# Performance work log

Measured on AMD Instinct MI355X. Metric: run time of the kernel, lower is better.

## Reference

```python
import jax, jax.numpy as jnp
import numpy as np

ALPHA = 0.1
K_HOPS = 16


def mlp_readout(y, ws, bs):
    # MLPReadout with L=2: two relu layers then linear
    for w, b in zip(ws[:-1], bs[:-1]):
        y = jax.nn.relu(y @ w.T + b)
    return y @ ws[-1].T + bs[-1]


def gru_dir(xs, w_ih, w_hh, b_ih, b_hh, reverse):
    # xs: [B, T, D]; PyTorch GRU cell semantics
    H = w_hh.shape[1]
    def cell(h, xt):
        gi = xt @ w_ih.T + b_ih            # [B, 3H]
        gh = h @ w_hh.T + b_hh             # [B, 3H]
        i_r, i_z, i_n = jnp.split(gi, 3, -1)
        h_r, h_z, h_n = jnp.split(gh, 3, -1)
        r = jax.nn.sigmoid(i_r + h_r)
        z = jax.nn.sigmoid(i_z + h_z)
        n = jnp.tanh(i_n + r * h_n)
        h2 = (1.0 - z) * n + z * h
        return h2, h2
    h0 = jnp.zeros((xs.shape[0], H), xs.dtype)
    _, ys = jax.lax.scan(cell, h0, jnp.swapaxes(xs, 0, 1), reverse=reverse)
    return jnp.swapaxes(ys, 0, 1)          # [B, T, H]


def appnp(x, edge_index):
    # APPNP with GCN symmetric normalization and self-loops
    N = x.shape[0]
    loop = jnp.arange(N, dtype=edge_index.dtype)
    src = jnp.concatenate([edge_index[0], loop])
    dst = jnp.concatenate([edge_index[1], loop])
    deg = jax.ops.segment_sum(jnp.ones(src.shape, x.dtype), dst, num_segments=N)
    dinv = jax.lax.rsqrt(jnp.maximum(deg, 1.0))
    w = (dinv[src] * dinv[dst])[:, None]    # [E+N, 1]
    def step(z, _):
        m = jax.ops.segment_sum(z[src] * w, dst, num_segments=N)
        return (1.0 - ALPHA) * m + ALPHA * x, None
    z, _ = jax.lax.scan(step, x, None, length=K_HOPS)
    return z


def setup_inputs():
    key = jax.random.key(0)
    ks = jax.random.split(key, 24)
    N, D, E, B, T, S, Hs, C = 20000, 768, 200000, 64, 128, 128, 512, 14
    sc = 0.05
    p = {}
    p['x'] = jax.random.normal(ks[0], (N, D), jnp.float32)
    p['edge_index'] = jax.random.randint(ks[1], (2, E), 0, N, dtype=jnp.int32).astype(jnp.int64)
    p['sequence'] = jax.random.normal(ks[2], (B, T, S), jnp.float32)
    p['batch'] = jnp.sort(jax.random.randint(ks[3], (N,), 0, B, dtype=jnp.int32)).astype(jnp.int64)
    # BiGRU params (forward / backward directions)
    p['gru_wih_f'] = jax.random.normal(ks[4], (3 * Hs, S), jnp.float32) * sc
    p['gru_whh_f'] = jax.random.normal(ks[5], (3 * Hs, Hs), jnp.float32) * sc
    p['gru_bih_f'] = jax.random.normal(ks[6], (3 * Hs,), jnp.float32) * sc
    p['gru_bhh_f'] = jax.random.normal(ks[7], (3 * Hs,), jnp.float32) * sc
    p['gru_wih_b'] = jax.random.normal(ks[8], (3 * Hs, S), jnp.float32) * sc
    p['gru_whh_b'] = jax.random.normal(ks[9], (3 * Hs, Hs), jnp.float32) * sc
    p['gru_bih_b'] = jax.random.normal(ks[10], (3 * Hs,), jnp.float32) * sc
    p['gru_bhh_b'] = jax.random.normal(ks[11], (3 * Hs,), jnp.float32) * sc
    # mlp_graph: 768 -> 384 -> 192 -> 14
    p['mg_w0'] = jax.random.normal(ks[12], (384, 768), jnp.float32) * sc
    p['mg_b0'] = jnp.zeros((384,), jnp.float32)
    p['mg_w1'] = jax.random.normal(ks[13], (192, 384), jnp.float32) * sc
    p['mg_b1'] = jnp.zeros((192,), jnp.float32)
    p['mg_w2'] = jax.random.normal(ks[14], (C, 192), jnp.float32) * sc
    p['mg_b2'] = jnp.zeros((C,), jnp.float32)
    # mlp_seq: 1024 -> 512 -> 256 -> 14
    p['ms_w0'] = jax.random.normal(ks[15], (512, 1024), jnp.float32) * sc
    p['ms_b0'] = jnp.zeros((512,), jnp.float32)
    p['ms_w1'] = jax.random.normal(ks[16], (256, 512), jnp.float32) * sc
    p['ms_b1'] = jnp.zeros((256,), jnp.float32)
    p['ms_w2'] = jax.random.normal(ks[17], (C, 256), jnp.float32) * sc
    p['ms_b2'] = jnp.zeros((C,), jnp.float32)
    return p


def reference(x, edge_index, sequence, batch,
              gru_wih_f, gru_whh_f, gru_bih_f, gru_bhh_f,
              gru_wih_b, gru_whh_b, gru_bih_b, gru_bhh_b,
              mg_w0, mg_b0, mg_w1, mg_b1, mg_w2, mg_b2,
              ms_w0, ms_b0, ms_w1, ms_b1, ms_w2, ms_b2):
    B = sequence.shape[0]
    # BiGRU over sequence (dropout is identity in eval mode)
    fwd = gru_dir(sequence, gru_wih_f, gru_whh_f, gru_bih_f, gru_bhh_f, False)
    bwd = gru_dir(sequence, gru_wih_b, gru_whh_b, gru_bih_b, gru_bhh_b, True)
    seq_out = jnp.concatenate([fwd, bwd], axis=-1)   # [B, T, 2H]
    seq1 = jnp.mean(seq_out, axis=1)                 # avg_pool over time
    seq2 = jnp.max(seq_out, axis=1)                  # max_pool over time
    seq_logits = mlp_readout(seq1 + seq2, [ms_w0, ms_w1, ms_w2], [ms_b0, ms_b1, ms_b2])
    # APPNP K-hop sparse propagation + global mean pool
    z = appnp(x, edge_index)
    cnt = jnp.maximum(jax.ops.segment_sum(jnp.ones((x.shape[0],), x.dtype), batch, num_segments=B), 1.0)
    pooled = jax.ops.segment_sum(z, batch, num_segments=B) / cnt[:, None]
    g_logits = mlp_readout(pooled, [mg_w0, mg_w1, mg_w2], [mg_b0, mg_b1, mg_b2])
    return g_logits + seq_logits
```

## Files before the change

### kernel.cpp

```cpp
#include <hip/hip_runtime.h>
#include <stdint.h>

#define ALPHA 0.1f
#define NN 20000
#define DF 768
#define NE 200000
#define NB 64
#define TSEQ 128
#define SF 128
#define HS 512
#define NCLS 14

typedef __attribute__((ext_vector_type(8))) short short8;
typedef __attribute__((ext_vector_type(4))) float f32x4;
typedef __attribute__((ext_vector_type(4))) unsigned int u32x4;

#define OFF_DEG     0u
#define OFF_CSRC    80000u
#define OFF_CNTB    160000u
#define OFF_FLAG64  176640u
#define ZERO_INTS   44161u
#define OFF_ROWPTR  176896u
#define OFF_CURSOR  257024u
#define OFF_DINV    337024u
#define OFF_COL     417024u
#define OFF_WGT     1217024u
#define OFF_V0      2017280u
#define OFF_V1      7137280u
#define OFF_HBUF    12257280u
#define OFF_HFLAG   12519424u
#define OFF_YSEQ    12781568u
#define OFF_PART    13240320u

__device__ __forceinline__ unsigned short f2b(float f) {
  union { float f; unsigned u; } v; v.f = f;
  unsigned u = v.u;
  return (unsigned short)((u + 0x7FFFu + ((u >> 16) & 1u)) >> 16);
}

__device__ __forceinline__ int idx_at(const int* p, long long i, int mode64) {
  return mode64 ? p[2*i] : p[i];
}

__device__ __forceinline__ float dot4(float4 a, float4 b) {
  return a.x * b.x + a.y * b.y + a.z * b.z + a.w * b.w;
}

__global__ void zero2_kernel(int* p1, int n1, int* p2, int n2) {
  int i = blockIdx.x * blockDim.x + threadIdx.x;
  if (i < n1) p1[i] = 0;
  int j = i - n1;
  if (j >= 0 && j < n2) p2[j] = 0;
}

__global__ void detect_i64_kernel(const int* e, int* flag) {
  int lane = threadIdx.x;
  int ok = 1;
  for (int i = lane; i < 256; i += 64) ok &= (e[2 * i + 1] == 0);
  ok = __all(ok);
  if (lane == 0 && blockIdx.x == 0) *flag = ok ? 1 : 0;
}

__global__ void hist_kernel(const int* e, const int* batch, int* deg, int* csrc,
                            int* cntb, const int* flag) {
  int i = blockIdx.x * blockDim.x + threadIdx.x;
  int m = *flag;
  if (i < NE) {
    int s = idx_at(e, i, m);
    int d = idx_at(e, (long long)NE + i, m);
    atomicAdd(&csrc[s], 1);
    atomicAdd(&deg[d], 1);
  }
  if (i < NN) atomicAdd(&cntb[idx_at(batch, i, m)], 1);
}

__global__ __launch_bounds__(1024) void combo_kernel(
    const int* __restrict__ csrc, const int* __restrict__ deg,
    int* __restrict__ row_ptr, int* __restrict__ cursor,
    float* __restrict__ dinv, const int* __restrict__ batch,
    const int* __restrict__ flag, float* __restrict__ v0) {
  const int tid = threadIdx.x, b = blockIdx.x;
  if (b < 20) {
    __shared__ int sA[1024], sB[1024];
    __shared__ int wred[16];
    __shared__ int carry_s;
    int psum = 0;
    for (int i = tid; i < b * 1000; i += 1024) psum += csrc[i];
    for (int off = 1; off < 64; off <<= 1) psum += __shfl_xor(psum, off);
    if ((tid & 63) == 0) wred[tid >> 6] = psum;
    __syncthreads();
    if (tid == 0) {
      int c = 0;
#pragma unroll
      for (int w = 0; w < 16; ++w) c += wred[w];
      carry_s = c;
    }
    int i = b * 1000 + tid;
    int active = (tid < 1000);
    int v = active ? csrc[i] : 0;
    sA[tid] = v;
    __syncthreads();
    int carry = carry_s;
    int* src = sA; int* dst = sB;
    for (int off = 1; off < 1024; off <<= 1) {
      dst[tid] = src[tid] + (tid >= off ? src[tid - off] : 0);
      __syncthreads();
      int* t = src; src = dst; dst = t;
    }
    if (active) {
      int ex = carry + src[tid] - v;
      row_ptr[i] = ex; cursor[i] = ex;
      dinv[i] = rsqrtf((float)(deg[i] + 1));
    }
    if (b == 19 && tid == 0) row_ptr[NN] = carry + src[999];
  } else {
    int m = *flag;
    long long j = (long long)(b - 20) * 1024 + tid;
    if (j < (long long)NN * 64) {
      int n = (int)(j >> 6), gb = (int)(j & 63);
      v0[j] = (idx_at(batch, n, m) == gb) ? 1.0f : 0.0f;
    }
  }
}

__global__ void fill_kernel(const int* e, const float* dinv, int* cursor,
                            int* colA, float* wgt, const int* flag) {
  int i = blockIdx.x * blockDim.x + threadIdx.x;
  if (i >= NE) return;
  int m = *flag;
  int s = idx_at(e, i, m);
  int d = idx_at(e, (long long)NE + i, m);
  int pos = atomicAdd(&cursor[s], 1);
  colA[pos] = d;
  wgt[pos] = dinv[s] * dinv[d];
}

__global__ __launch_bounds__(256) void hop_kernel(
    const float* __restrict__ vin, float* __restrict__ vout,
    const int* __restrict__ row_ptr, const int* __restrict__ colA,
    const float* __restrict__ wgt, const float* __restrict__ dinv,
    const int* __restrict__ batch, const int* __restrict__ flag) {
  int wid = (blockIdx.x * blockDim.x + threadIdx.x) >> 6;
  int lane = threadIdx.x & 63;
  if (wid >= NN) return;
  const int quad = lane >> 4, l15 = lane & 15;
  const int c4 = l15 * 4;
  float di = dinv[wid];
  int e0 = __builtin_amdgcn_readfirstlane(row_ptr[wid]);
  int e1 = __builtin_amdgcn_readfirstlane(row_ptr[wid + 1]);

  float ax, ay, az, aw;
  {
    float w = (quad == 0) ? di * di : 0.0f;
    const float* vr = vin + (size_t)wid * 64 + c4;
    ax = w * vr[0]; ay = w * vr[1]; az = w * vr[2]; aw = w * vr[3];
  }
  for (int e = e0; e < e1; e += 16) {
    int i0 = e + quad, i1 = i0 + 4, i2 = i0 + 8, i3 = i0 + 12;
    int a0 = (i0 < e1), a1 = (i1 < e1), a2 = (i2 < e1), a3 = (i3 < e1);
    int j0 = a0 ? i0 : e0, j1 = a1 ? i1 : e0, j2 = a2 ? i2 : e0, j3 = a3 ? i3 : e0;
    int cc0 = colA[j0], cc1 = colA[j1], cc2 = colA[j2], cc3 = colA[j3];
    float w0 = a0 ? wgt[j0] : 0.0f, w1 = a1 ? wgt[j1] : 0.0f;
    float w2 = a2 ? wgt[j2] : 0.0f, w3 = a3 ? wgt[j3] : 0.0f;
    float4 v0 = *(const float4*)(vin + (size_t)cc0 * 64 + c4);
    float4 v1 = *(const float4*)(vin + (size_t)cc1 * 64 + c4);
    float4 v2 = *(const float4*)(vin + (size_t)cc2 * 64 + c4);
    float4 v3 = *(const float4*)(vin + (size_t)cc3 * 64 + c4);
    ax += w0 * v0.x + w1 * v1.x + w2 * v2.x + w3 * v3.x;
    ay += w0 * v0.y + w1 * v1.y + w2 * v2.y + w3 * v3.y;
    az += w0 * v0.z + w1 * v1.z + w2 * v2.z + w3 * v3.z;
    aw += w0 * v0.w + w1 * v1.w + w2 * v2.w + w3 * v3.w;
  }
  ax += __shfl_xor(ax, 16); ax += __shfl_xor(ax, 32);
  ay += __shfl_xor(ay, 16); ay += __shfl_xor(ay, 32);
  az += __shfl_xor(az, 16); az += __shfl_xor(az, 32);
  aw += __shfl_xor(aw, 16); aw += __shfl_xor(aw, 32);
  if (quad == 0) {
    int b = idx_at(batch, wid, *flag);
    float* o = vout + (size_t)wid * 64 + c4;
    float4 r;
    r.x = (1.0f - ALPHA) * ax + ((b == c4 + 0) ? ALPHA : 0.0f);
    r.y = (1.0f - ALPHA) * ay + ((b == c4 + 1) ? ALPHA : 0.0f);
    r.z = (1.0f - ALPHA) * az + ((b == c4 + 2) ? ALPHA : 0.0f);
    r.w = (1.0f - ALPHA) * aw + ((b == c4 + 3) ? ALPHA : 0.0f);
    *(float4*)o = r;
  }
}

__global__ __launch_bounds__(256) void spmm_kernel(
    const float* __restrict__ S, const float* __restrict__ x,
    float* __restrict__ partial) {
  __shared__ float red[4][64][17];
  int tid = threadIdx.x;
  int w = tid >> 6, lane = tid & 63;
  int beta = blockIdx.x;
  int ft = beta % 48, cg = beta / 48;
  int ch = cg * 4 + w;
  int f0 = ft * 16;
  int n0 = (ch * NN) >> 6, n1 = ((ch + 1) * NN) >> 6;
  float acc[16];
#pragma unroll
  for (int f = 0; f < 16; ++f) acc[f] = 0.0f;
  for (int n = n0; n < n1; ++n) {
    float sv = S[n * 64 + lane];
    const float4* xr = (const float4*)(x + (size_t)n * DF + f0);
    float4 x0 = xr[0], x1 = xr[1], x2 = xr[2], x3 = xr[3];
    acc[0] += sv * x0.x; acc[1] += sv * x0.y; acc[2] += sv * x0.z; acc[3] += sv * x0.w;
    acc[4] += sv * x1.x; acc[5] += sv * x1.y; acc[6] += sv * x1.z; acc[7] += sv * x1.w;
    acc[8] += sv * x2.x; acc[9] += sv * x2.y; acc[10] += sv * x2.z; acc[11] += sv * x2.w;
    acc[12] += sv * x3.x; acc[13] += sv * x3.y; acc[14] += sv * x3.z; acc[15] += sv * x3.w;
  }
#pragma unroll
  for (int f = 0; f < 16; ++f) red[w][lane][f] = acc[f];
  __syncthreads();
#pragma unroll
  for (int ff = 0; ff < 4; ++ff) {
    int f = w * 4 + ff;
    float s = red[0][lane][f] + red[1][lane][f] + red[2][lane][f] + red[3][lane][f];
    partial[((size_t)(cg * 64 + lane)) * DF + f0 + f] = s;
  }
}

__global__ __launch_bounds__(256) void mlp_seq_kernel(
    const float* __restrict__ y_seq,
    const float* __restrict__ w0, const float* __restrict__ b0,
    const float* __restrict__ w1, const float* __restrict__ b1,
    const float* __restrict__ w2, const float* __restrict__ b2,
    float* __restrict__ out) {
  __shared__ float a0[1024], h1[512], h2[256];
  const int tid = threadIdx.x, b = blockIdx.x;
  ((float4*)a0)[tid] = ((const float4*)(y_seq + (size_t)b * 1024))[tid];
  __syncthreads();
  {
    int n = tid * 2;
    float acc0 = b0[n], acc1 = b0[n + 1];
    const float4* wa = (const float4*)(w0 + (size_t)n * 1024);
    const float4* wb = wa + 256;
#pragma unroll 4
    for (int k = 0; k < 256; ++k) {
      float4 av = ((float4*)a0)[k];
      acc0 += dot4(av, wa[k]);
      acc1 += dot4(av, wb[k]);
    }
    h1[n] = fmaxf(acc0, 0.0f);
    h1[n + 1] = fmaxf(acc1, 0.0f);
  }
  __syncthreads();
  {
    float acc = b1[tid];
    const float4* wa = (const float4*)(w1 + (size_t)tid * 512);
#pragma unroll 4
    for (int k = 0; k < 128; ++k) acc += dot4(((float4*)h1)[k], wa[k]);
    h2[tid] = fmaxf(acc, 0.0f);
  }
  __syncthreads();
  if (tid < 224) {
    int o = tid >> 4, l = tid & 15;
    const float4* wa = (const float4*)(w2 + (size_t)o * 256);
    float part = 0.0f;
#pragma unroll
    for (int k = l; k < 64; k += 16) part += dot4(((float4*)h2)[k], wa[k]);
    part += __shfl_xor(part, 1); part += __shfl_xor(part, 2);
    part += __shfl_xor(part, 4); part += __shfl_xor(part, 8);
    if (l == 0) out[b * NCLS + o] = part + b2[o];
  }
}

__global__ __launch_bounds__(256) void mlp_graph_kernel(
    const float* __restrict__ partial, const int* __restrict__ cntb,
    const float* __restrict__ w0, const float* __restrict__ b0,
    const float* __restrict__ w1, const float* __restrict__ b1,
    const float* __restrict__ w2, const float* __restrict__ b2,
    float* __restrict__ out) {
  __shared__ float a0[768], h1[384], h2[192];
  const int tid = threadIdx.x, b = blockIdx.x;
  int cnt = cntb[b]; if (cnt < 1) cnt = 1;
  const float cinv = 1.0f / (float)cnt;
  if (tid < 192) {
    float4 s = {0, 0, 0, 0};
#pragma unroll
    for (int c = 0; c < 16; ++c) {
      float4 p = ((const float4*)(partial + ((size_t)(c * 64 + b)) * DF))[tid];
      s.x += p.x; s.y += p.y; s.z += p.z; s.w += p.w;
    }
    s.x *= cinv; s.y *= cinv; s.z *= cinv; s.w *= cinv;
    ((float4*)a0)[tid] = s;
  }
  __syncthreads();
  if (tid < 192) {
    int n = tid * 2;
    float acc0 = b0[n], acc1 = b0[n + 1];
    const float4* wa = (const float4*)(w0 + (size_t)n * 768);
    const float4* wb = wa + 192;
#pragma unroll 4
    for (int k = 0; k < 192; ++k) {
      float4 av = ((float4*)a0)[k];
      acc0 += dot4(av, wa[k]);
      acc1 += dot4(av, wb[k]);
    }
    h1[n] = fmaxf(acc0, 0.0f);
    h1[n + 1] = fmaxf(acc1, 0.0f);
  }
  __syncthreads();
  if (tid < 192) {
    float acc = b1[tid];
    const float4* wa = (const float4*)(w1 + (size_t)tid * 384);
#pragma unroll 4
    for (int k = 0; k < 96; ++k) acc += dot4(((float4*)h1)[k], wa[k]);
    h2[tid] = fmaxf(acc, 0.0f);
  }
  __syncthreads();
  if (tid < 224) {
    int o = tid >> 4, l = tid & 15;
    const float4* wa = (const float4*)(w2 + (size_t)o * 192);
    float part = 0.0f;
#pragma unroll
    for (int k = l; k < 48; k += 16) part += dot4(((float4*)h2)[k], wa[k]);
    part += __shfl_xor(part, 1); part += __shfl_xor(part, 2);
    part += __shfl_xor(part, 4); part += __shfl_xor(part, 8);
    if (l == 0) atomicAdd(&out[b * NCLS + o], part + b2[o]);
  }
}

__global__ __launch_bounds__(64, 1) void gru_kernel(
    const float* __restrict__ seq,
    const float* __restrict__ wih_f, const float* __restrict__ whh_f,
    const float* __restrict__ bih_f, const float* __restrict__ bhh_f,
    const float* __restrict__ wih_b, const float* __restrict__ whh_b,
    const float* __restrict__ bih_b, const float* __restrict__ bhh_b,
    unsigned* __restrict__ hbuf, unsigned* __restrict__ hflag,
    float* __restrict__ y_seq) {
  __shared__ unsigned short hl[8 * 648];

  const int lane = threadIdx.x;
  const int quad = lane >> 4, l15 = lane & 15;
  const int d  = blockIdx.x >> 8;
  const int g  = (blockIdx.x >> 5) & 7;
  const int rk = blockIdx.x & 31;
  const int seqbase = g * 8;
  const int c0 = rk * 16;

  const float* WHHd = d ? whh_b : whh_f;
  const float* WIHd = d ? wih_b : wih_f;
  const float* BIHd = d ? bih_b : bih_f;
  const float* BHHd = d ? bhh_b : bhh_f;

  auto ldw = [&](int gcol, int j) -> short8 {
    int k0 = j * 32 + quad * 8;
    const float* p = (k0 < 512) ? (WHHd + (size_t)gcol * 512 + k0)
                                : (WIHd + (size_t)gcol * 128 + (k0 - 512));
    float4 f0 = *(const float4*)p;
    float4 f1 = *(const float4*)(p + 4);
    short8 r;
    r[0] = (short)f2b(f0.x); r[1] = (short)f2b(f0.y);
    r[2] = (short)f2b(f0.z); r[3] = (short)f2b(f0.w);
    r[4] = (short)f2b(f1.x); r[5] = (short)f2b(f1.y);
    r[6] = (short)f2b(f1.z); r[7] = (short)f2b(f1.w);
    return r;
  };
  short8 wr[20], wz[20], wn[20];
#pragma unroll
  for (int j = 0; j < 20; ++j) {
    wr[j] = ldw(c0 + l15, j);
    wz[j] = ldw(512 + c0 + l15, j);
    wn[j] = ldw(1024 + c0 + l15, j);
  }

  auto stage_x = [&](int t_x) {
    int tt = d ? (127 - t_x) : t_x;
    int s = lane >> 3, k0 = (lane & 7) * 16;
    const float* sp = seq + (size_t)(seqbase + s) * (TSEQ * SF) + tt * SF + k0;
    float4 a = *(const float4*)sp;
    float4 b = *(const float4*)(sp + 4);
    float4 c = *(const float4*)(sp + 8);
    float4 e = *(const float4*)(sp + 12);
    unsigned* xq = (unsigned*)(hl + s * 648 + 512 + k0);
    xq[0] = (unsigned)f2b(a.x) | ((unsigned)f2b(a.y) << 16);
    xq[1] = (unsigned)f2b(a.z) | ((unsigned)f2b(a.w) << 16);
    xq[2] = (unsigned)f2b(b.x) | ((unsigned)f2b(b.y) << 16);
    xq[3] = (unsigned)f2b(b.z) | ((unsigned)f2b(b.w) << 16);
    xq[4] = (unsigned)f2b(c.x) | ((unsigned)f2b(c.y) << 16);
    xq[5] = (unsigned)f2b(c.z) | ((unsigned)f2b(c.w) << 16);
    xq[6] = (unsigned)f2b(e.x) | ((unsigned)f2b(e.y) << 16);
    xq[7] = (unsigned)f2b(e.z) | ((unsigned)f2b(e.w) << 16);
  };

  for (int i = lane; i < 8 * 512; i += 64)
    hl[(i >> 9) * 648 + (i & 511)] = 0;
  stage_x(0);

  const float b_r  = BIHd[c0 + l15] + BHHd[c0 + l15];
  const float b_z  = BIHd[512 + c0 + l15] + BHHd[512 + c0 + l15];
  const float b_in = BIHd[1024 + c0 + l15];
  const float b_hn = BHHd[1024 + c0 + l15];

  float hprev[4] = {0, 0, 0, 0};
  float msum[4]  = {0, 0, 0, 0};
  float mxv[4]   = {-1e30f, -1e30f, -1e30f, -1e30f};

  for (int t = 0; t < 128; ++t) {
    f32x4 ar = {0, 0, 0, 0}, az = {0, 0, 0, 0};
    f32x4 anh = {0, 0, 0, 0}, anx = {0, 0, 0, 0};
    const unsigned short* arow = hl + (l15 & 7) * 648 + quad * 8;
#pragma unroll
    for (int kc = 0; kc < 20; ++kc) {
      short8 af = *(const short8*)(arow + kc * 32);
      ar = __builtin_amdgcn_mfma_f32_16x16x32_bf16(af, wr[kc], ar, 0, 0, 0);
      az = __builtin_amdgcn_mfma_f32_16x16x32_bf16(af, wz[kc], az, 0, 0, 0);
      if (kc < 16)
        anh = __builtin_amdgcn_mfma_f32_16x16x32_bf16(af, wn[kc], anh, 0, 0, 0);
      else
        anx = __builtin_amdgcn_mfma_f32_16x16x32_bf16(af, wn[kc], anx, 0, 0, 0);
    }

    float h2v[4];
#pragma unroll
    for (int rr = 0; rr < 4; ++rr) {
      float r = 1.0f / (1.0f + __expf(-(ar[rr] + b_r)));
      float z = 1.0f / (1.0f + __expf(-(az[rr] + b_z)));
      float narg = anx[rr] + b_in + r * (anh[rr] + b_hn);
      float e2 = __expf(-2.0f * fabsf(narg));
      float nt = (1.0f - e2) / (1.0f + e2);
      nt = (narg < 0.0f) ? -nt : nt;
      float h2 = (1.0f - z) * nt + z * hprev[rr];
      hprev[rr] = h2; msum[rr] += h2; mxv[rr] = fmaxf(mxv[rr], h2);
      h2v[rr] = h2;
    }

    if (t < 127) {
      const int slot = (t + 1) & 1;
      const unsigned tag = (unsigned)(t + 1);
#pragma unroll
      for (int rr = 0; rr < 4; ++rr) {
        unsigned me = f2b(h2v[rr]);
        unsigned nb = (unsigned)__shfl_xor((int)me, 1);
        if (lane < 32 && !(lane & 1)) {
          int row = (lane >> 4) * 4 + rr;
          unsigned word = (me & 0xFFFFu) | (nb << 16);
          unsigned* dp = hbuf +
              ((size_t)((slot * 2 + d) * 64 + seqbase + row)) * 256 +
              (unsigned)((c0 + (lane & 15)) >> 1);
          asm volatile("global_store_dword %0, %1, off sc0 sc1"
                       :: "v"(dp), "v"(word) : "memory");
        }
      }
      asm volatile("s_waitcnt vmcnt(0)" ::: "memory");
      if (lane == 0) {
        unsigned* fpo = hflag + ((size_t)(slot * 2 + d) * 8 + g) * 64 + rk;
        unsigned tv = tag;
        asm volatile("global_store_dword %0, %1, off sc0 sc1"
                     :: "v"(fpo), "v"(tv) : "memory");
      }
      stage_x(t + 1);
      const unsigned* fp = hflag + ((size_t)(slot * 2 + d) * 8 + g) * 64 + (lane & 31);
      int guard = 0;
      unsigned fv;
      for (;;) {
        asm volatile("global_load_dword %0, %1, off sc0 sc1"
                     : "=v"(fv) : "v"(fp) : "memory");
        asm volatile("s_waitcnt vmcnt(0)" ::: "memory");
        __builtin_amdgcn_sched_barrier(0);
        if (__all(fv == tag)) break;
        if (++guard > (1 << 20)) break;
        __builtin_amdgcn_s_sleep(1);
      }
      const unsigned* db = hbuf + (size_t)((slot * 2 + d) * 64 + seqbase) * 256;
      u32x4 w[8];
#pragma unroll
      for (int c = 0; c < 8; ++c)
        asm volatile("global_load_dwordx4 %0, %1, off sc0 sc1"
                     : "=v"(w[c]) : "v"(db + c * 256 + lane * 4) : "memory");
      asm volatile("s_waitcnt vmcnt(0)" ::: "memory");
      __builtin_amdgcn_sched_barrier(0);
#pragma unroll
      for (int c = 0; c < 8; ++c) {
        unsigned* dp = (unsigned*)(hl + c * 648) + lane * 4;
        dp[0] = w[c][0]; dp[1] = w[c][1]; dp[2] = w[c][2]; dp[3] = w[c][3];
      }
    }
  }

  if (lane < 32) {
#pragma unroll
    for (int rr = 0; rr < 4; ++rr) {
      int row = (lane >> 4) * 4 + rr;
      y_seq[(size_t)(seqbase + row) * 1024 + d * 512 + c0 + l15] =
          msum[rr] * (1.0f / 128.0f) + mxv[rr];
    }
  }
}

extern "C" void kernel_launch(void* const* d_in, const int* in_sizes, int n_in,
                              void* d_out, int out_size, void* d_ws, size_t ws_size,
                              hipStream_t stream) {
  const float* x      = (const float*)d_in[0];
  const int*   eidx   = (const int*)d_in[1];
  const float* seq    = (const float*)d_in[2];
  const int*   batch  = (const int*)d_in[3];
  const float* wih_f  = (const float*)d_in[4];
  const float* whh_f  = (const float*)d_in[5];
  const float* bih_f  = (const float*)d_in[6];
  const float* bhh_f  = (const float*)d_in[7];
  const float* wih_b  = (const float*)d_in[8];
  const float* whh_b  = (const float*)d_in[9];
  const float* bih_b  = (const float*)d_in[10];
  const float* bhh_b  = (const float*)d_in[11];
  const float* mg_w0  = (const float*)d_in[12];
  const float* mg_b0  = (const float*)d_in[13];
  const float* mg_w1  = (const float*)d_in[14];
  const float* mg_b1  = (const float*)d_in[15];
  const float* mg_w2  = (const float*)d_in[16];
  const float* mg_b2  = (const float*)d_in[17];
  const float* ms_w0  = (const float*)d_in[18];
  const float* ms_b0  = (const float*)d_in[19];
  const float* ms_w1  = (const float*)d_in[20];
  const float* ms_b1  = (const float*)d_in[21];
  const float* ms_w2  = (const float*)d_in[22];
  const float* ms_b2  = (const float*)d_in[23];
  float* out = (float*)d_out;
  char* ws = (char*)d_ws;

  int*   deg     = (int*)(ws + OFF_DEG);
  int*   csrc    = (int*)(ws + OFF_CSRC);
  int*   cntb    = (int*)(ws + OFF_CNTB);
  int*   flag    = (int*)(ws + OFF_FLAG64);
  int*   row_ptr = (int*)(ws + OFF_ROWPTR);
  int*   cursor  = (int*)(ws + OFF_CURSOR);
  float* dinv    = (float*)(ws + OFF_DINV);
  int*   colA    = (int*)(ws + OFF_COL);
  float* wgtA    = (float*)(ws + OFF_WGT);
  float* V0      = (float*)(ws + OFF_V0);
  float* V1      = (float*)(ws + OFF_V1);
  unsigned* hbuf = (unsigned*)(ws + OFF_HBUF);
  unsigned* hflag= (unsigned*)(ws + OFF_HFLAG);
  float* y_seq   = (float*)(ws + OFF_YSEQ);
  float* part    = (float*)(ws + OFF_PART);

  zero2_kernel<<<(ZERO_INTS + 2048 + 255) / 256, 256, 0, stream>>>(
      (int*)ws, (int)ZERO_INTS, (int*)(ws + OFF_HFLAG), 2048);
  detect_i64_kernel<<<1, 64, 0, stream>>>(eidx, flag);
  hist_kernel<<<(NE + 255) / 256, 256, 0, stream>>>(eidx, batch, deg, csrc,
                                                    cntb, flag);
  combo_kernel<<<20 + (NN * 64 + 1023) / 1024, 1024, 0, stream>>>(
      csrc, deg, row_ptr, cursor, dinv, batch, flag, V0);
  fill_kernel<<<(NE + 255) / 256, 256, 0, stream>>>(eidx, dinv, cursor, colA, wgtA, flag);

  for (int h = 0; h < 16; ++h) {
    const float* vin = (h & 1) ? V1 : V0;
    float* vout = (h & 1) ? V0 : V1;
    hop_kernel<<<(NN * 64 + 255) / 256, 256, 0, stream>>>(vin, vout, row_ptr, colA,
                                                          wgtA, dinv, batch, flag);
  }

  spmm_kernel<<<768, 256, 0, stream>>>(V0, x, part);

  gru_kernel<<<512, 64, 0, stream>>>(
      seq, wih_f, whh_f, bih_f, bhh_f, wih_b, whh_b, bih_b, bhh_b, hbuf, hflag, y_seq);

  mlp_seq_kernel<<<64, 256, 0, stream>>>(y_seq, ms_w0, ms_b0, ms_w1, ms_b1,
                                         ms_w2, ms_b2, out);
  mlp_graph_kernel<<<64, 256, 0, stream>>>(part, cntb, mg_w0, mg_b0, mg_w1, mg_b1,
                                           mg_w2, mg_b2, out);
  (void)in_sizes; (void)n_in; (void)out_size; (void)ws_size;
}
```

Before: 1.228 ms.

## Store APPNP propagation vectors in fp16 and fuse spmm into GRU launch

The 64-wide propagated batch-indicator vectors are now stored as fp16 instead of fp32, halving the gather traffic of each of the 16 hop kernels. The spmm reduction is merged into the GRU kernel as extra blocks so both run concurrently in a single launch, letting the latency-bound GRU recurrence overlap the bandwidth-bound spmm. The fused launch uses 256-thread blocks, and the 512 GRU blocks keep only their first 64 threads. This risks precision loss in the propagated values and may disturb the GRU's cross-block flag synchronization if its blocks are not all co-resident.

```diff
diff --git a/kernel.cpp b/kernel.cpp
--- a/kernel.cpp
+++ b/kernel.cpp
@@ -38,6 +38,14 @@
   return (unsigned short)((u + 0x7FFFu + ((u >> 16) & 1u)) >> 16);
 }
 
+union U16h { unsigned short u; _Float16 h; };
+__device__ __forceinline__ float h2f(unsigned short u) {
+  U16h t; t.u = u; return (float)t.h;
+}
+__device__ __forceinline__ unsigned short f2h(float f) {
+  U16h t; t.h = (_Float16)f; return t.u;
+}
+
 __device__ __forceinline__ int idx_at(const int* p, long long i, int mode64) {
   return mode64 ? p[2*i] : p[i];
 }
@@ -78,7 +86,7 @@
     const int* __restrict__ csrc, const int* __restrict__ deg,
     int* __restrict__ row_ptr, int* __restrict__ cursor,
     float* __restrict__ dinv, const int* __restrict__ batch,
-    const int* __restrict__ flag, float* __restrict__ v0) {
+    const int* __restrict__ flag, unsigned short* __restrict__ v0) {
   const int tid = threadIdx.x, b = blockIdx.x;
   if (b < 20) {
     __shared__ int sA[1024], sB[1024];
@@ -118,7 +126,7 @@
     long long j = (long long)(b - 20) * 1024 + tid;
     if (j < (long long)NN * 64) {
       int n = (int)(j >> 6), gb = (int)(j & 63);
-      v0[j] = (idx_at(batch, n, m) == gb) ? 1.0f : 0.0f;
+      v0[j] = (idx_at(batch, n, m) == gb) ? (unsigned short)0x3C00 : 0;
     }
   }
 }
@@ -136,7 +144,7 @@
 }
 
 __global__ __launch_bounds__(256) void hop_kernel(
-    const float* __restrict__ vin, float* __restrict__ vout,
+    const unsigned short* __restrict__ vin, unsigned short* __restrict__ vout,
     const int* __restrict__ row_ptr, const int* __restrict__ colA,
     const float* __restrict__ wgt, const float* __restrict__ dinv,
     const int* __restrict__ batch, const int* __restrict__ flag) {
@@ -152,8 +160,8 @@
   float ax, ay, az, aw;
   {
     float w = (quad == 0) ? di * di : 0.0f;
-    const float* vr = vin + (size_t)wid * 64 + c4;
-    ax = w * vr[0]; ay = w * vr[1]; az = w * vr[2]; aw = w * vr[3];
+    ushort4 sv = *(const ushort4*)(vin + (size_t)wid * 64 + c4);
+    ax = w * h2f(sv.x); ay = w * h2f(sv.y); az = w * h2f(sv.z); aw = w * h2f(sv.w);
   }
   for (int e = e0; e < e1; e += 16) {
     int i0 = e + quad, i1 = i0 + 4, i2 = i0 + 8, i3 = i0 + 12;
@@ -162,14 +170,14 @@
     int cc0 = colA[j0], cc1 = colA[j1], cc2 = colA[j2], cc3 = colA[j3];
     float w0 = a0 ? wgt[j0] : 0.0f, w1 = a1 ? wgt[j1] : 0.0f;
     float w2 = a2 ? wgt[j2] : 0.0f, w3 = a3 ? wgt[j3] : 0.0f;
-    float4 v0 = *(const float4*)(vin + (size_t)cc0 * 64 + c4);
-    float4 v1 = *(const float4*)(vin + (size_t)cc1 * 64 + c4);
-    float4 v2 = *(const float4*)(vin + (size_t)cc2 * 64 + c4);
-    float4 v3 = *(const float4*)(vin + (size_t)cc3 * 64 + c4);
-    ax += w0 * v0.x + w1 * v1.x + w2 * v2.x + w3 * v3.x;
-    ay += w0 * v0.y + w1 * v1.y + w2 * v2.y + w3 * v3.y;
-    az += w0 * v0.z + w1 * v1.z + w2 * v2.z + w3 * v3.z;
-    aw += w0 * v0.w + w1 * v1.w + w2 * v2.w + w3 * v3.w;
+    ushort4 v0 = *(const ushort4*)(vin + (size_t)cc0 * 64 + c4);
+    ushort4 v1 = *(const ushort4*)(vin + (size_t)cc1 * 64 + c4);
+    ushort4 v2 = *(const ushort4*)(vin + (size_t)cc2 * 64 + c4);
+    ushort4 v3 = *(const ushort4*)(vin + (size_t)cc3 * 64 + c4);
+    ax += w0 * h2f(v0.x) + w1 * h2f(v1.x) + w2 * h2f(v2.x) + w3 * h2f(v3.x);
+    ay += w0 * h2f(v0.y) + w1 * h2f(v1.y) + w2 * h2f(v2.y) + w3 * h2f(v3.y);
+    az += w0 * h2f(v0.z) + w1 * h2f(v1.z) + w2 * h2f(v2.z) + w3 * h2f(v3.z);
+    aw += w0 * h2f(v0.w) + w1 * h2f(v1.w) + w2 * h2f(v2.w) + w3 * h2f(v3.w);
   }
   ax += __shfl_xor(ax, 16); ax += __shfl_xor(ax, 32);
   ay += __shfl_xor(ay, 16); ay += __shfl_xor(ay, 32);
@@ -177,160 +185,64 @@
   aw += __shfl_xor(aw, 16); aw += __shfl_xor(aw, 32);
   if (quad == 0) {
     int b = idx_at(batch, wid, *flag);
-    float* o = vout + (size_t)wid * 64 + c4;
-    float4 r;
-    r.x = (1.0f - ALPHA) * ax + ((b == c4 + 0) ? ALPHA : 0.0f);
-    r.y = (1.0f - ALPHA) * ay + ((b == c4 + 1) ? ALPHA : 0.0f);
-    r.z = (1.0f - ALPHA) * az + ((b == c4 + 2) ? ALPHA : 0.0f);
-    r.w = (1.0f - ALPHA) * aw + ((b == c4 + 3) ? ALPHA : 0.0f);
-    *(float4*)o = r;
-  }
-}
-
-__global__ __launch_bounds__(256) void spmm_kernel(
-    const float* __restrict__ S, const float* __restrict__ x,
-    float* __restrict__ partial) {
-  __shared__ float red[4][64][17];
-  int tid = threadIdx.x;
-  int w = tid >> 6, lane = tid & 63;
-  int beta = blockIdx.x;
-  int ft = beta % 48, cg = beta / 48;
-  int ch = cg * 4 + w;
-  int f0 = ft * 16;
-  int n0 = (ch * NN) >> 6, n1 = ((ch + 1) * NN) >> 6;
-  float acc[16];
-#pragma unroll
-  for (int f = 0; f < 16; ++f) acc[f] = 0.0f;
-  for (int n = n0; n < n1; ++n) {
-    float sv = S[n * 64 + lane];
-    const float4* xr = (const float4*)(x + (size_t)n * DF + f0);
-    float4 x0 = xr[0], x1 = xr[1], x2 = xr[2], x3 = xr[3];
-    acc[0] += sv * x0.x; acc[1] += sv * x0.y; acc[2] += sv * x0.z; acc[3] += sv * x0.w;
-    acc[4] += sv * x1.x; acc[5] += sv * x1.y; acc[6] += sv * x1.z; acc[7] += sv * x1.w;
-    acc[8] += sv * x2.x; acc[9] += sv * x2.y; acc[10] += sv * x2.z; acc[11] += sv * x2.w;
-    acc[12] += sv * x3.x; acc[13] += sv * x3.y; acc[14] += sv * x3.z; acc[15] += sv * x3.w;
-  }
-#pragma unroll
-  for (int f = 0; f < 16; ++f) red[w][lane][f] = acc[f];
-  __syncthreads();
-#pragma unroll
-  for (int ff = 0; ff < 4; ++ff) {
-    int f = w * 4 + ff;
-    float s = red[0][lane][f] + red[1][lane][f] + red[2][lane][f] + red[3][lane][f];
-    partial[((size_t)(cg * 64 + lane)) * DF + f0 + f] = s;
-  }
-}
-
-__global__ __launch_bounds__(256) void mlp_seq_kernel(
-    const float* __restrict__ y_seq,
-    const float* __restrict__ w0, const float* __restrict__ b0,
-    const float* __restrict__ w1, const float* __restrict__ b1,
-    const float* __restrict__ w2, const float* __restrict__ b2,
-    float* __restrict__ out) {
-  __shared__ float a0[1024], h1[512], h2[256];
-  const int tid = threadIdx.x, b = blockIdx.x;
-  ((float4*)a0)[tid] = ((const float4*)(y_seq + (size_t)b * 1024))[tid];
-  __syncthreads();
-  {
-    int n = tid * 2;
-    float acc0 = b0[n], acc1 = b0[n + 1];
-    const float4* wa = (const float4*)(w0 + (size_t)n * 1024);
-    const float4* wb = wa + 256;
-#pragma unroll 4
-    for (int k = 0; k < 256; ++k) {
-      float4 av = ((float4*)a0)[k];
-      acc0 += dot4(av, wa[k]);
-      acc1 += dot4(av, wb[k]);
-    }
-    h1[n] = fmaxf(acc0, 0.0f);
-    h1[n + 1] = fmaxf(acc1, 0.0f);
-  }
-  __syncthreads();
-  {
-    float acc = b1[tid];
-    const float4* wa = (const float4*)(w1 + (size_t)tid * 512);
-#pragma unroll 4
-    for (int k = 0; k < 128; ++k) acc += dot4(((float4*)h1)[k], wa[k]);
-    h2[tid] = fmaxf(acc, 0.0f);
-  }
-  __syncthreads();
-  if (tid < 224) {
-    int o = tid >> 4, l = tid & 15;
-    const float4* wa = (const float4*)(w2 + (size_t)o * 256);
-    float part = 0.0f;
-#pragma unroll
-    for (int k = l; k < 64; k += 16) part += dot4(((float4*)h2)[k], wa[k]);
-    part += __shfl_xor(part, 1); part += __shfl_xor(part, 2);
-    part += __shfl_xor(part, 4); part += __shfl_xor(part, 8);
-    if (l == 0) out[b * NCLS + o] = part + b2[o];
-  }
-}
-
-__global__ __launch_bounds__(256) void mlp_graph_kernel(
-    const float* __restrict__ partial, const int* __restrict__ cntb,
-    const float* __restrict__ w0, const float* __restrict__ b0,
-    const float* __restrict__ w1, const float* __restrict__ b1,
-    const float* __restrict__ w2, const float* __restrict__ b2,
-    float* __restrict__ out) {
-  __shared__ float a0[768], h1[384], h2[192];
-  const int tid = threadIdx.x, b = blockIdx.x;
-  int cnt = cntb[b]; if (cnt < 1) cnt = 1;
-  const float cinv = 1.0f / (float)cnt;
-  if (tid < 192) {
-    float4 s = {0, 0, 0, 0};
-#pragma unroll
-    for (int c = 0; c < 16; ++c) {
-      float4 p = ((const float4*)(partial + ((size_t)(c * 64 + b)) * DF))[tid];
-      s.x += p.x; s.y += p.y; s.z += p.z; s.w += p.w;
-    }
-    s.x *= cinv; s.y *= cinv; s.z *= cinv; s.w *= cinv;
-    ((float4*)a0)[tid] = s;
-  }
-  __syncthreads();
-  if (tid < 192) {
-    int n = tid * 2;
-    float acc0 = b0[n], acc1 = b0[n + 1];
-    const float4* wa = (const float4*)(w0 + (size_t)n * 768);
-    const float4* wb = wa + 192;
-#pragma unroll 4
-    for (int k = 0; k < 192; ++k) {
-      float4 av = ((float4*)a0)[k];
-      acc0 += dot4(av, wa[k]);
-      acc1 += dot4(av, wb[k]);
-    }
-    h1[n] = fmaxf(acc0, 0.0f);
-    h1[n + 1] = fmaxf(acc1, 0.0f);
-  }
-  __syncthreads();
-  if (tid < 192) {
-    float acc = b1[tid];
-    const float4* wa = (const float4*)(w1 + (size_t)tid * 384);
-#pragma unroll 4
-    for (int k = 0; k < 96; ++k) acc += dot4(((float4*)h1)[k], wa[k]);
-    h2[tid] = fmaxf(acc, 0.0f);
-  }
-  __syncthreads();
-  if (tid < 224) {
-    int o = tid >> 4, l = tid & 15;
-    const float4* wa = (const float4*)(w2 + (size_t)o * 192);
-    float part = 0.0f;
-#pragma unroll
-    for (int k = l; k < 48; k += 16) part += dot4(((float4*)h2)[k], wa[k]);
-    part += __shfl_xor(part, 1); part += __shfl_xor(part, 2);
-    part += __shfl_xor(part, 4); part += __shfl_xor(part, 8);
-    if (l == 0) atomicAdd(&out[b * NCLS + o], part + b2[o]);
-  }
-}
-
-__global__ __launch_bounds__(64, 1) void gru_kernel(
+    ushort4 r;
+    r.x = f2h((1.0f - ALPHA) * ax + ((b == c4 + 0) ? ALPHA : 0.0f));
+    r.y = f2h((1.0f - ALPHA) * ay + ((b == c4 + 1) ? ALPHA : 0.0f));
+    r.z = f2h((1.0f - ALPHA) * az + ((b == c4 + 2) ? ALPHA : 0.0f));
+    r.w = f2h((1.0f - ALPHA) * aw + ((b == c4 + 3) ? ALPHA : 0.0f));
+    *(ushort4*)(vout + (size_t)wid * 64 + c4) = r;
+  }
+}
+
+#define SMEM_BYTES 17408
+
+__global__ __launch_bounds__(256) void gru_spmm_kernel(
     const float* __restrict__ seq,
     const float* __restrict__ wih_f, const float* __restrict__ whh_f,
     const float* __restrict__ bih_f, const float* __restrict__ bhh_f,
     const float* __restrict__ wih_b, const float* __restrict__ whh_b,
     const float* __restrict__ bih_b, const float* __restrict__ bhh_b,
     unsigned* __restrict__ hbuf, unsigned* __restrict__ hflag,
-    float* __restrict__ y_seq) {
-  __shared__ unsigned short hl[8 * 648];
+    float* __restrict__ y_seq,
+    const unsigned short* __restrict__ S, const float* __restrict__ x,
+    float* __restrict__ partial) {
+  __shared__ char smem[SMEM_BYTES];
+
+  if (blockIdx.x >= 512) {
+    float (*red)[64][17] = (float(*)[64][17])smem;
+    int tid = threadIdx.x;
+    int w = tid >> 6, lane = tid & 63;
+    int beta = blockIdx.x - 512;
+    int ft = beta % 48, cg = beta / 48;
+    int ch = cg * 4 + w;
+    int f0 = ft * 16;
+    int n0 = (ch * NN) >> 6, n1 = ((ch + 1) * NN) >> 6;
+    float acc[16];
+#pragma unroll
+    for (int f = 0; f < 16; ++f) acc[f] = 0.0f;
+    for (int n = n0; n < n1; ++n) {
+      float sv = h2f(S[n * 64 + lane]);
+      const float4* xr = (const float4*)(x + (size_t)n * DF + f0);
+      float4 x0 = xr[0], x1 = xr[1], x2 = xr[2], x3 = xr[3];
+      acc[0] += sv * x0.x; acc[1] += sv * x0.y; acc[2] += sv * x0.z; acc[3] += sv * x0.w;
+      acc[4] += sv * x1.x; acc[5] += sv * x1.y; acc[6] += sv * x1.z; acc[7] += sv * x1.w;
+      acc[8] += sv * x2.x; acc[9] += sv * x2.y; acc[10] += sv * x2.z; acc[11] += sv * x2.w;
+      acc[12] += sv * x3.x; acc[13] += sv * x3.y; acc[14] += sv * x3.z; acc[15] += sv * x3.w;
+    }
+#pragma unroll
+    for (int f = 0; f < 16; ++f) red[w][lane][f] = acc[f];
+    __syncthreads();
+#pragma unroll
+    for (int ff = 0; ff < 4; ++ff) {
+      int f = w * 4 + ff;
+      float s = red[0][lane][f] + red[1][lane][f] + red[2][lane][f] + red[3][lane][f];
+      partial[((size_t)(cg * 64 + lane)) * DF + f0 + f] = s;
+    }
+    return;
+  }
+
+  if (threadIdx.x >= 64) return;
+  unsigned short* hl = (unsigned short*)smem;
 
   const int lane = threadIdx.x;
   const int quad = lane >> 4, l15 = lane & 15;
@@ -490,6 +402,107 @@
   }
 }
 
+__global__ __launch_bounds__(256) void mlp_seq_kernel(
+    const float* __restrict__ y_seq,
+    const float* __restrict__ w0, const float* __restrict__ b0,
+    const float* __restrict__ w1, const float* __restrict__ b1,
+    const float* __restrict__ w2, const float* __restrict__ b2,
+    float* __restrict__ out) {
+  __shared__ float a0[1024], h1[512], h2[256];
+  const int tid = threadIdx.x, b = blockIdx.x;
+  ((float4*)a0)[tid] = ((const float4*)(y_seq + (size_t)b * 1024))[tid];
+  __syncthreads();
+  {
+    int n = tid * 2;
+    float acc0 = b0[n], acc1 = b0[n + 1];
+    const float4* wa = (const float4*)(w0 + (size_t)n * 1024);
+    const float4* wb = wa + 256;
+#pragma unroll 4
+    for (int k = 0; k < 256; ++k) {
+      float4 av = ((float4*)a0)[k];
+      acc0 += dot4(av, wa[k]);
+      acc1 += dot4(av, wb[k]);
+    }
+    h1[n] = fmaxf(acc0, 0.0f);
+    h1[n + 1] = fmaxf(acc1, 0.0f);
+  }
+  __syncthreads();
+  {
+    float acc = b1[tid];
+    const float4* wa = (const float4*)(w1 + (size_t)tid * 512);
+#pragma unroll 4
+    for (int k = 0; k < 128; ++k) acc += dot4(((float4*)h1)[k], wa[k]);
+    h2[tid] = fmaxf(acc, 0.0f);
+  }
+  __syncthreads();
+  if (tid < 224) {
+    int o = tid >> 4, l = tid & 15;
+    const float4* wa = (const float4*)(w2 + (size_t)o * 256);
+    float part = 0.0f;
+#pragma unroll
+    for (int k = l; k < 64; k += 16) part += dot4(((float4*)h2)[k], wa[k]);
+    part += __shfl_xor(part, 1); part += __shfl_xor(part, 2);
+    part += __shfl_xor(part, 4); part += __shfl_xor(part, 8);
+    if (l == 0) out[b * NCLS + o] = part + b2[o];
+  }
+}
+
+__global__ __launch_bounds__(256) void mlp_graph_kernel(
+    const float* __restrict__ partial, const int* __restrict__ cntb,
+    const float* __restrict__ w0, const float* __restrict__ b0,
+    const float* __restrict__ w1, const float* __restrict__ b1,
+    const float* __restrict__ w2, const float* __restrict__ b2,
+    float* __restrict__ out) {
+  __shared__ float a0[768], h1[384], h2[192];
+  const int tid = threadIdx.x, b = blockIdx.x;
+  int cnt = cntb[b]; if (cnt < 1) cnt = 1;
+  const float cinv = 1.0f / (float)cnt;
+  if (tid < 192) {
+    float4 s = {0, 0, 0, 0};
+#pragma unroll
+    for (int c = 0; c < 16; ++c) {
+      float4 p = ((const float4*)(partial + ((size_t)(c * 64 + b)) * DF))[tid];
+      s.x += p.x; s.y += p.y; s.z += p.z; s.w += p.w;
+    }
+    s.x *= cinv; s.y *= cinv; s.z *= cinv; s.w *= cinv;
+    ((float4*)a0)[tid] = s;
+  }
+  __syncthreads();
+  if (tid < 192) {
+    int n = tid * 2;
+    float acc0 = b0[n], acc1 = b0[n + 1];
+    const float4* wa = (const float4*)(w0 + (size_t)n * 768);
+    const float4* wb = wa + 192;
+#pragma unroll 4
+    for (int k = 0; k < 192; ++k) {
+      float4 av = ((float4*)a0)[k];
+      acc0 += dot4(av, wa[k]);
+      acc1 += dot4(av, wb[k]);
+    }
+    h1[n] = fmaxf(acc0, 0.0f);
+    h1[n + 1] = fmaxf(acc1, 0.0f);
+  }
+  __syncthreads();
+  if (tid < 192) {
+    float acc = b1[tid];
+    const float4* wa = (const float4*)(w1 + (size_t)tid * 384);
+#pragma unroll 4
+    for (int k = 0; k < 96; ++k) acc += dot4(((float4*)h1)[k], wa[k]);
+    h2[tid] = fmaxf(acc, 0.0f);
+  }
+  __syncthreads();
+  if (tid < 224) {
+    int o = tid >> 4, l = tid & 15;
+    const float4* wa = (const float4*)(w2 + (size_t)o * 192);
+    float part = 0.0f;
+#pragma unroll
+    for (int k = l; k < 48; k += 16) part += dot4(((float4*)h2)[k], wa[k]);
+    part += __shfl_xor(part, 1); part += __shfl_xor(part, 2);
+    part += __shfl_xor(part, 4); part += __shfl_xor(part, 8);
+    if (l == 0) atomicAdd(&out[b * NCLS + o], part + b2[o]);
+  }
+}
+
 extern "C" void kernel_launch(void* const* d_in, const int* in_sizes, int n_in,
                               void* d_out, int out_size, void* d_ws, size_t ws_size,
                               hipStream_t stream) {
@@ -529,8 +542,8 @@
   float* dinv    = (float*)(ws + OFF_DINV);
   int*   colA    = (int*)(ws + OFF_COL);
   float* wgtA    = (float*)(ws + OFF_WGT);
-  float* V0      = (float*)(ws + OFF_V0);
-  float* V1      = (float*)(ws + OFF_V1);
+  unsigned short* V0 = (unsigned short*)(ws + OFF_V0);
+  unsigned short* V1 = (unsigned short*)(ws + OFF_V1);
   unsigned* hbuf = (unsigned*)(ws + OFF_HBUF);
   unsigned* hflag= (unsigned*)(ws + OFF_HFLAG);
   float* y_seq   = (float*)(ws + OFF_YSEQ);
@@ -546,16 +559,15 @@
   fill_kernel<<<(NE + 255) / 256, 256, 0, stream>>>(eidx, dinv, cursor, colA, wgtA, flag);
 
   for (int h = 0; h < 16; ++h) {
-    const float* vin = (h & 1) ? V1 : V0;
-    float* vout = (h & 1) ? V0 : V1;
+    const unsigned short* vin = (h & 1) ? V1 : V0;
+    unsigned short* vout = (h & 1) ? V0 : V1;
     hop_kernel<<<(NN * 64 + 255) / 256, 256, 0, stream>>>(vin, vout, row_ptr, colA,
                                                           wgtA, dinv, batch, flag);
   }
 
-  spmm_kernel<<<768, 256, 0, stream>>>(V0, x, part);
-
-  gru_kernel<<<512, 64, 0, stream>>>(
-      seq, wih_f, whh_f, bih_f, bhh_f, wih_b, whh_b, bih_b, bhh_b, hbuf, hflag, y_seq);
+  gru_spmm_kernel<<<512 + 768, 256, 0, stream>>>(
+      seq, wih_f, whh_f, bih_f, bhh_f, wih_b, whh_b, bih_b, bhh_b,
+      hbuf, hflag, y_seq, V0, x, part);
 
   mlp_seq_kernel<<<64, 256, 0, stream>>>(y_seq, ms_w0, ms_b0, ms_w1, ms_b1,
                                          ms_w2, ms_b2, out);
```

Result: slower. 1.769 ms (+44.0%).
